# Kernel optimization log

Measured on AMD Instinct MI355X. Metric: run time of the kernel, lower is better.

Reference implementation:

```python
import jax, jax.numpy as jnp
import numpy as np

D = 768
H = 8
HD = D // H
MLP = 3072
EPS = 1e-5


def _ln(x, g, b):
    mu = jnp.mean(x, axis=-1, keepdims=True)
    var = jnp.var(x, axis=-1, keepdims=True)
    return (x - mu) * jax.lax.rsqrt(var + EPS) * g + b


def setup_inputs() -> dict:
    key = jax.random.key(0)
    ks = jax.random.split(key, 20)
    B, N = 4, 2048
    s = 0.02
    inp = {
        "x": jax.random.normal(ks[0], (B, N, D), jnp.float32),
        "position_bias": jax.random.normal(ks[1], (N, N), jnp.float32),
        "wq": jax.random.normal(ks[2], (D, D), jnp.float32) * s,
        "bq": jnp.zeros((D,), jnp.float32),
        "wk": jax.random.normal(ks[3], (D, D), jnp.float32) * s,
        "bk": jnp.zeros((D,), jnp.float32),
        "wv": jax.random.normal(ks[4], (D, D), jnp.float32) * s,
        "bv": jnp.zeros((D,), jnp.float32),
        "wo": jax.random.normal(ks[5], (D, D), jnp.float32) * s,
        "bo": jnp.zeros((D,), jnp.float32),
        "g1": jnp.ones((D,), jnp.float32),
        "b1": jnp.zeros((D,), jnp.float32),
        "g2": jnp.ones((D,), jnp.float32),
        "b2": jnp.zeros((D,), jnp.float32),
        "w_ff1": jax.random.normal(ks[6], (D, MLP), jnp.float32) * s,
        "b_ff1": jnp.zeros((MLP,), jnp.float32),
        "w_ff2": jax.random.normal(ks[7], (MLP, D), jnp.float32) * s,
        "b_ff2": jnp.zeros((D,), jnp.float32),
    }
    return inp


def reference(x, position_bias, wq, bq, wk, bk, wv, bv, wo, bo, g1, b1, g2, b2, w_ff1, b_ff1, w_ff2, b_ff2):
    B, N, _ = x.shape
    scale = HD ** -0.5
    # pre-norm attention
    n1 = _ln(x, g1, b1)
    q = (n1 @ wq + bq).reshape(B, N, H, HD).transpose(0, 2, 1, 3)
    k = (n1 @ wk + bk).reshape(B, N, H, HD).transpose(0, 2, 1, 3)
    v = (n1 @ wv + bv).reshape(B, N, H, HD).transpose(0, 2, 1, 3)
    attn = jnp.einsum('bhqd,bhkd->bhqk', q, k) * scale  # [B,H,N,N]
    attn = attn + position_bias[None, None, :, :]
    attn = jax.nn.softmax(attn, axis=-1)
    out = jnp.einsum('bhqk,bhkd->bhqd', attn, v)
    out = out.transpose(0, 2, 1, 3).reshape(B, N, D)
    out = out @ wo + bo
    x = x + out
    # pre-norm GELU MLP (exact erf gelu, torch default)
    n2 = _ln(x, g2, b2)
    h = jax.nn.gelu(n2 @ w_ff1 + b_ff1, approximate=False)
    x = x + (h @ w_ff2 + b_ff2)
    return x
```

## Files before the change

kernel.cpp:

```cpp
#include <hip/hip_runtime.h>
#include <hip/hip_bf16.h>

#define D 768
#define H 8
#define HD 96
#define MLP 3072
#define NB 2048
#define BATCH 4

typedef __attribute__((ext_vector_type(8))) short short8;
typedef __attribute__((ext_vector_type(4))) short short4v;
typedef __attribute__((ext_vector_type(4))) float f32x4;
typedef __attribute__((ext_vector_type(16))) float f32x16;
typedef __attribute__((ext_vector_type(4))) int int4v;

typedef const __attribute__((address_space(1))) unsigned int gu32;
typedef __attribute__((address_space(3))) unsigned int lu32;

__device__ inline void gload16(const void* g, void* l){
  __builtin_amdgcn_global_load_lds((gu32*)g, (lu32*)l, 16, 0, 0);
}

__device__ inline short f2b(float f){
  __hip_bfloat16 h = __float2bfloat16(f);
  return *reinterpret_cast<short*>(&h);
}
__device__ inline float b2f(short s){
  return __uint_as_float(((unsigned)(unsigned short)s) << 16);
}
__device__ inline float fexp2(float x){ return __builtin_amdgcn_exp2f(x); }

__device__ inline unsigned cvtpk(float lo, float hi){
  unsigned r;
  asm volatile("v_cvt_pk_bf16_f32 %0, %1, %2" : "=v"(r) : "v"(lo), "v"(hi));
  return r;
}

__global__ __launch_bounds__(256) void wtrans(const float* __restrict__ in, short* __restrict__ out, int K, int Nc){
  __shared__ float tile[32][33];
  int bk = blockIdx.x, bn = blockIdx.y;
  int tx = threadIdx.x & 31, ty = threadIdx.x >> 5;
  #pragma unroll
  for (int i=0;i<4;++i)
    tile[ty + i*8][tx] = in[(size_t)(bk*32 + ty + i*8)*Nc + bn*32 + tx];
  __syncthreads();
  #pragma unroll
  for (int i=0;i<4;++i)
    out[(size_t)(bn*32 + ty + i*8)*K + bk*32 + tx] = f2b(tile[tx][ty + i*8]);
}

__global__ __launch_bounds__(256) void bias_cat(const float* __restrict__ bq, const float* __restrict__ bk,
                                                const float* __restrict__ bv, float* __restrict__ o){
  int i = blockIdx.x*256 + threadIdx.x;
  if (i < 768){ o[i]=bq[i]; o[768+i]=bk[i]; o[1536+i]=bv[i]; }
}

__global__ __launch_bounds__(256) void pb_reorg(const float* __restrict__ pb, short* __restrict__ pbT){
  int qt = blockIdx.x, kb = blockIdx.y;
  int t = threadIdx.x;
  int l = t >> 2;
  int vbase = (t & 3) * 8;
  int q = qt*32 + (l & 31);
  int hi = l >> 5;
  const float L2E = 1.4426950408889634f;
  short8 o;
  #pragma unroll
  for (int j=0;j<8;++j){
    int v = vbase + j;
    int r = v & 15, tile = v >> 4;
    int k = kb*64 + tile*32 + 8*(r>>2) + (r&3) + 4*hi;
    o[j] = f2b(pb[(size_t)q*NB + k] * L2E);
  }
  *(short8*)&pbT[(((size_t)(qt*32 + kb))*64 + l)*32 + vbase] = o;
}

__global__ __launch_bounds__(256) void ln_k(const float* __restrict__ X, const float* __restrict__ gg,
                                            const float* __restrict__ bb, short* __restrict__ out){
  int row = blockIdx.x, t = threadIdx.x;
  const float* x = X + (size_t)row*D;
  float v0=x[t], v1=x[t+256], v2=x[t+512];
  float s=v0+v1+v2, ss=v0*v0+v1*v1+v2*v2;
  #pragma unroll
  for (int m=1;m<64;m<<=1){ s += __shfl_xor(s,m); ss += __shfl_xor(ss,m); }
  __shared__ float red[8];
  int w=t>>6, lane=t&63;
  if (!lane){ red[w]=s; red[4+w]=ss; }
  __syncthreads();
  s = red[0]+red[1]+red[2]+red[3];
  ss = red[4]+red[5]+red[6]+red[7];
  float mu = s*(1.f/768.f);
  float inv = rsqrtf(ss*(1.f/768.f) - mu*mu + 1e-5f);
  short* o = out + (size_t)row*D;
  o[t]     = f2b((v0-mu)*inv*gg[t]     + bb[t]);
  o[t+256] = f2b((v1-mu)*inv*gg[t+256] + bb[t+256]);
  o[t+512] = f2b((v2-mu)*inv*gg[t+512] + bb[t+512]);
}

template<int MODE>
__global__ __launch_bounds__(256) void gemm_bt(
    const short* __restrict__ A, const short* __restrict__ Bt,
    const float* __restrict__ bias, const float* __restrict__ resid,
    void* __restrict__ Cout, int Nc, int K)
{
  __shared__ __align__(16) short As[3][128][32];
  __shared__ __align__(16) short Bs[3][128][32];
  int m0 = blockIdx.x*128, n0 = blockIdx.y*128;
  int t = threadIdx.x;
  int lane = t & 63, w = t >> 6;
  int wm = w >> 1, wn = w & 1;
  int r = lane & 15, g = lane >> 4;
  const short* aSrc = A  + (size_t)(m0 + (t>>2))*K + (t&3)*8;
  const short* bSrc = Bt + (size_t)(n0 + (t>>2))*K + (t&3)*8;
  size_t rowK64 = (size_t)64*K;
  int dstOff = w*1024;
  f32x4 acc[4][4] = {};
  int nst = K >> 5;
  auto stage = [&](int u, int buf){
    char* ab = (char*)As + buf*8192;
    char* bb = (char*)Bs + buf*8192;
    int kt = u*32;
    gload16(aSrc + kt,          ab + dstOff);
    gload16(aSrc + kt + rowK64, ab + 4096 + dstOff);
    gload16(bSrc + kt,          bb + dstOff);
    gload16(bSrc + kt + rowK64, bb + 4096 + dstOff);
  };
  stage(0,0); stage(1,1);
  int cur = 0;
  for (int it=0; it<nst; ++it){
    if (it < nst-1) asm volatile("s_waitcnt vmcnt(4)" ::: "memory");
    else            asm volatile("s_waitcnt vmcnt(0)" ::: "memory");
    __builtin_amdgcn_s_barrier();
    __builtin_amdgcn_sched_barrier(0);
    if (it+2 < nst){
      int sb = cur+2; if (sb>=3) sb-=3;
      stage(it+2, sb);
    }
    short8 af[4], bfr[4];
    #pragma unroll
    for (int i=0;i<4;++i){
      af[i]  = *(const short8*)&As[cur][wm*64 + i*16 + r][g*8];
      bfr[i] = *(const short8*)&Bs[cur][wn*64 + i*16 + r][g*8];
    }
    #pragma unroll
    for (int i=0;i<4;++i)
      #pragma unroll
      for (int j=0;j<4;++j)
        acc[i][j] = __builtin_amdgcn_mfma_f32_16x16x32_bf16(af[i], bfr[j], acc[i][j], 0,0,0);
    cur = cur+1; if (cur>=3) cur-=3;
  }
  #pragma unroll
  for (int i=0;i<4;++i){
    #pragma unroll
    for (int j=0;j<4;++j){
      int col = n0 + wn*64 + j*16 + r;
      float bv = bias[col];
      #pragma unroll
      for (int q=0;q<4;++q){
        int row = m0 + wm*64 + i*16 + g*4 + q;
        size_t idx = (size_t)row*Nc + col;
        float val = acc[i][j][q] + bv;
        if constexpr (MODE==0){
          ((short*)Cout)[idx] = f2b(val);
        } else if constexpr (MODE==2){
          float ge = 0.5f*val*(1.f + erff(val*0.70710678118654752f));
          ((short*)Cout)[idx] = f2b(ge);
        }
      }
    }
  }
}

template<int MODE>
__global__ __launch_bounds__(256) void gemm64(
    const short* __restrict__ A, const short* __restrict__ Bt,
    const float* __restrict__ bias, const float* __restrict__ resid,
    void* __restrict__ Cout, int Nc, int K)
{
  __shared__ __align__(16) short As[3][64][32];
  __shared__ __align__(16) short Bs[3][128][32];
  int m0 = blockIdx.x*64, n0 = blockIdx.y*128;
  int t = threadIdx.x;
  int lane = t & 63, w = t >> 6;
  int r = lane & 15, g = lane >> 4;
  const short* aSrc = A  + (size_t)(m0 + (t>>2))*K + (t&3)*8;
  const short* bSrc = Bt + (size_t)(n0 + (t>>2))*K + (t&3)*8;
  size_t rowK64 = (size_t)64*K;
  int dstOff = w*1024;
  f32x4 acc[4][2] = {};
  int nst = K >> 5;
  auto stage = [&](int u, int buf){
    char* ab = (char*)As + buf*4096;
    char* bb = (char*)Bs + buf*8192;
    int kt = u*32;
    gload16(aSrc + kt,          ab + dstOff);
    gload16(bSrc + kt,          bb + dstOff);
    gload16(bSrc + kt + rowK64, bb + 4096 + dstOff);
  };
  stage(0,0); stage(1,1);
  int cur = 0;
  for (int it=0; it<nst; ++it){
    if (it < nst-1) asm volatile("s_waitcnt vmcnt(3)" ::: "memory");
    else            asm volatile("s_waitcnt vmcnt(0)" ::: "memory");
    __builtin_amdgcn_s_barrier();
    __builtin_amdgcn_sched_barrier(0);
    if (it+2 < nst){
      int sb = cur+2; if (sb>=3) sb-=3;
      stage(it+2, sb);
    }
    short8 af[4], bfr[2];
    #pragma unroll
    for (int i=0;i<4;++i) af[i] = *(const short8*)&As[cur][i*16 + r][g*8];
    #pragma unroll
    for (int j=0;j<2;++j) bfr[j] = *(const short8*)&Bs[cur][w*32 + j*16 + r][g*8];
    #pragma unroll
    for (int i=0;i<4;++i)
      #pragma unroll
      for (int j=0;j<2;++j)
        acc[i][j] = __builtin_amdgcn_mfma_f32_16x16x32_bf16(af[i], bfr[j], acc[i][j], 0,0,0);
    cur = cur+1; if (cur>=3) cur-=3;
  }
  #pragma unroll
  for (int i=0;i<4;++i){
    #pragma unroll
    for (int j=0;j<2;++j){
      int col = n0 + w*32 + j*16 + r;
      #pragma unroll
      for (int q=0;q<4;++q){
        int row = m0 + i*16 + g*4 + q;
        if constexpr (MODE==1){
          size_t idx = (size_t)row*Nc + col;
          ((float*)Cout)[idx] = acc[i][j][q] + bias[col] + resid[idx];
        } else {
          int hh = row / 96, hd = row - hh*96;
          int bb = col >> 11, nn = col & 2047;
          size_t idx = ((size_t)((bb*8 + hh)*96 + hd))*2048 + nn;
          ((short*)Cout)[idx] = f2b(acc[i][j][q] + bias[row]);
        }
      }
    }
  }
}

__global__ __launch_bounds__(512, 1) void attn_k(const short* __restrict__ qkv, const short* __restrict__ v_t,
                                                 const short* __restrict__ pbT, short* __restrict__ aout){
  int bx = blockIdx.x;
  int h = bx & 7, b = (bx>>3)&3, qb = bx>>5;
  int t = threadIdx.x, l = t & 63, w = t >> 6;
  int l31 = l & 31, hi = l >> 5, l7 = l & 7;
  __shared__ __align__(16) short Ks[2][64][128];
  __shared__ __align__(16) short Vs[2][96][64];
  const float SCALE2 = 0.10206207261596575f * 1.4426950408889634f;

  int qRow = qb*256 + w*32 + l31;
  const short* qg = qkv + (size_t)(b*NB + qRow)*1536 + h*HD;
  short8 qa[6];
  #pragma unroll
  for (int ds=0; ds<6; ++ds)
    qa[ds] = *(const short8*)&qg[ds*16 + hi*8];

  f32x16 oacc[3] = {};
  float m_run = -3.0e38f, l_run = 0.f;

  int r0 = t/12,        c0 = t%12;
  int s1 = 512 + t;
  int r1 = s1/12,       c1 = s1%12;
  int ldsK0 = r0*128 + (c0 ^ (r0&7))*8;
  int ldsK1 = r1*128 + (c1 ^ (r1&7))*8;
  const short* kgB = qkv + (size_t)(b*NB)*1536 + 768 + h*HD;
  bool wlow = (t < 256);
  int vr0 = t>>3,  vc0 = t&7;
  int vr1 = (512+t)>>3, vc1 = (512+t)&7;
  const short* vgB = v_t + (size_t)((b*H+h)*HD)*NB;
  const short* vsrc0 = vgB + (size_t)vr0*NB + (vc0 ^ (vr0&7))*8;
  const short* vsrc1 = vgB + (size_t)vr1*NB + (vc1 ^ (vr1&7))*8;
  const short* pbB = pbT + (((size_t)((qb*8 + w)*32))*64 + l)*32;

  {
    short8 ka = *(const short8*)&kgB[(size_t)r0*1536 + c0*8];
    short* ks0 = &Ks[0][0][0];
    *(short8*)(ks0 + ldsK0) = ka;
    if (wlow){
      short8 kb = *(const short8*)&kgB[(size_t)r1*1536 + c1*8];
      *(short8*)(ks0 + ldsK1) = kb;
    }
    gload16(vsrc0, (char*)Vs + w*1024);
    if (wlow) gload16(vsrc1, (char*)Vs + 8192 + w*1024);
  }
  __syncthreads();

  for (int kt=0; kt<32; ++kt){
    int cur = kt & 1;
    int kbase = kt*64;
    int kb2 = (kt < 31) ? (kbase + 64) : kbase;
    short8 kra = *(const short8*)&kgB[(size_t)(kb2 + r0)*1536 + c0*8];
    short8 krb = {};
    if (wlow) krb = *(const short8*)&kgB[(size_t)(kb2 + r1)*1536 + c1*8];
    const short* pbk = pbB + kt*2048;
    short8 pbr0 = *(const short8*)&pbk[0];
    short8 pbr1 = *(const short8*)&pbk[8];
    short8 pbr2 = *(const short8*)&pbk[16];
    short8 pbr3 = *(const short8*)&pbk[24];
    if (kt < 31){
      char* vbd = (char*)Vs + (cur^1)*12288;
      gload16(vsrc0 + kbase + 64, vbd + w*1024);
      if (wlow) gload16(vsrc1 + kbase + 64, vbd + 8192 + w*1024);
    }

    f32x16 sacc[2] = {};
    __builtin_amdgcn_s_setprio(1);
    #pragma unroll
    for (int tt=0; tt<2; ++tt){
      #pragma unroll
      for (int ds=0; ds<6; ++ds){
        short8 kf = *(const short8*)&Ks[cur][tt*32 + l31][((ds*2 + hi) ^ l7)*8];
        sacc[tt] = __builtin_amdgcn_mfma_f32_32x32x16_bf16(kf, qa[ds], sacc[tt], 0,0,0);
      }
    }
    __builtin_amdgcn_s_setprio(0);

    float vals[2][16];
    #pragma unroll
    for (int tt=0; tt<2; ++tt)
      #pragma unroll
      for (int r=0; r<16; ++r){
        int v = tt*16 + r;
        short pv = (v<8)?pbr0[v]:(v<16)?pbr1[v-8]:(v<24)?pbr2[v-16]:pbr3[v-24];
        vals[tt][r] = fmaf(sacc[tt][r], SCALE2, b2f(pv));
      }
    float pm = vals[0][0];
    #pragma unroll
    for (int tt=0; tt<2; ++tt)
      #pragma unroll
      for (int r=0; r<16; ++r) pm = fmaxf(pm, vals[tt][r]);
    pm = fmaxf(pm, __shfl_xor(pm, 32));
    if (__any(pm - m_run > 8.f)){
      float mn = fmaxf(m_run, pm);
      float f = fexp2(m_run - mn);
      l_run *= f; m_run = mn;
      int fi = __float_as_int(f);
      #pragma unroll
      for (int reg=0; reg<16; ++reg){
        int q = (reg&3) + 8*(reg>>2) + 4*hi;
        float fr = __int_as_float(__builtin_amdgcn_ds_bpermute(q<<2, fi));
        oacc[0][reg] *= fr; oacc[1][reg] *= fr; oacc[2][reg] *= fr;
      }
    }
    float p[2][16];
    float rs = 0.f;
    #pragma unroll
    for (int tt=0; tt<2; ++tt)
      #pragma unroll
      for (int r=0; r<16; ++r){
        p[tt][r] = fexp2(vals[tt][r] - m_run);
        rs += p[tt][r];
      }
    rs += __shfl_xor(rs, 32);
    l_run += rs;

    short8 pa[4];
    #pragma unroll
    for (int ks=0; ks<4; ++ks){
      int tt = ks>>1;
      int rb = (ks&1)*8;
      unsigned G0a = cvtpk(p[tt][rb+0], p[tt][rb+1]);
      unsigned G0b = cvtpk(p[tt][rb+2], p[tt][rb+3]);
      unsigned G1a = cvtpk(p[tt][rb+4], p[tt][rb+5]);
      unsigned G1b = cvtpk(p[tt][rb+6], p[tt][rb+7]);
      unsigned sG0a = (unsigned)__shfl_xor((int)G0a, 32);
      unsigned sG0b = (unsigned)__shfl_xor((int)G0b, 32);
      unsigned sG1a = (unsigned)__shfl_xor((int)G1a, 32);
      unsigned sG1b = (unsigned)__shfl_xor((int)G1b, 32);
      int4v wv;
      wv[0] = hi ? (int)sG1a : (int)G0a;
      wv[1] = hi ? (int)sG1b : (int)G0b;
      wv[2] = hi ? (int)G1a  : (int)sG0a;
      wv[3] = hi ? (int)G1b  : (int)sG0b;
      pa[ks] = __builtin_bit_cast(short8, wv);
    }

    __builtin_amdgcn_s_setprio(1);
    #pragma unroll
    for (int dt=0; dt<3; ++dt){
      #pragma unroll
      for (int ks=0; ks<4; ++ks){
        short8 vb = *(const short8*)&Vs[cur][dt*32 + l31][((ks*2 + hi) ^ l7)*8];
        oacc[dt] = __builtin_amdgcn_mfma_f32_32x32x16_bf16(pa[ks], vb, oacc[dt], 0,0,0);
      }
    }
    __builtin_amdgcn_s_setprio(0);

    if (kt < 31){
      short* ksn = &Ks[cur^1][0][0];
      *(short8*)(ksn + ldsK0) = kra;
      if (wlow) *(short8*)(ksn + ldsK1) = krb;
      __syncthreads();
    }
  }

  float inv_self = 1.f / l_run;
  int ii = __float_as_int(inv_self);
  #pragma unroll
  for (int reg=0; reg<16; ++reg){
    int q = (reg&3) + 8*(reg>>2) + 4*hi;
    float invq = __int_as_float(__builtin_amdgcn_ds_bpermute(q<<2, ii));
    int rowg = b*NB + qb*256 + w*32 + q;
    #pragma unroll
    for (int dt=0; dt<3; ++dt){
      int col = h*HD + dt*32 + l31;
      aout[(size_t)rowg*D + col] = f2b(oacc[dt][reg] * invq);
    }
  }
}

extern "C" void kernel_launch(void* const* d_in, const int* in_sizes, int n_in,
                              void* d_out, int out_size, void* d_ws, size_t ws_size,
                              hipStream_t stream){
  const float* x   = (const float*)d_in[0];
  const float* pb  = (const float*)d_in[1];
  const float* wq  = (const float*)d_in[2];
  const float* bq  = (const float*)d_in[3];
  const float* wk  = (const float*)d_in[4];
  const float* bk  = (const float*)d_in[5];
  const float* wv  = (const float*)d_in[6];
  const float* bv  = (const float*)d_in[7];
  const float* wo  = (const float*)d_in[8];
  const float* bo  = (const float*)d_in[9];
  const float* g1  = (const float*)d_in[10];
  const float* b1  = (const float*)d_in[11];
  const float* g2  = (const float*)d_in[12];
  const float* b2  = (const float*)d_in[13];
  const float* wf1 = (const float*)d_in[14];
  const float* bf1 = (const float*)d_in[15];
  const float* wf2 = (const float*)d_in[16];
  const float* bf2 = (const float*)d_in[17];
  float* out = (float*)d_out;

  char* p = (char*)d_ws;
  auto alloc = [&](size_t bytes){ char* q = p; p += (bytes + 255) & ~(size_t)255; return q; };
  short* wqkv_t = (short*)alloc((size_t)2304*768*2);
  short* wo_t   = (short*)alloc((size_t)768*768*2);
  short* w1_t   = (short*)alloc((size_t)3072*768*2);
  short* w2_t   = (short*)alloc((size_t)768*3072*2);
  float* bqkv   = (float*)alloc(2304*4);
  short* pbT    = (short*)alloc((size_t)2048*2048*2);
  float* x1     = (float*)alloc((size_t)8192*768*4);
  short* n2     = (short*)alloc((size_t)8192*768*2);
  short* n1     = (short*)alloc((size_t)8192*768*2);
  short* qkv    = (short*)alloc((size_t)8192*1536*2);
  short* v_t    = (short*)alloc((size_t)32*96*2048*2);
  short* hbuf   = n1;
  short* attn_o = n1;
  short* wv_t   = wqkv_t + (size_t)2*768*768;

  wtrans<<<dim3(24,24),256,0,stream>>>(wq, wqkv_t,           768, 768);
  wtrans<<<dim3(24,24),256,0,stream>>>(wk, wqkv_t + 768*768, 768, 768);
  wtrans<<<dim3(24,24),256,0,stream>>>(wv, wv_t,             768, 768);
  wtrans<<<dim3(24,24),256,0,stream>>>(wo, wo_t, 768, 768);
  wtrans<<<dim3(24,96),256,0,stream>>>(wf1, w1_t, 768, 3072);
  wtrans<<<dim3(96,24),256,0,stream>>>(wf2, w2_t, 3072, 768);
  bias_cat<<<3,256,0,stream>>>(bq,bk,bv,bqkv);
  pb_reorg<<<dim3(64,32),256,0,stream>>>(pb, pbT);
  ln_k<<<8192,256,0,stream>>>(x, g1, b1, n1);
  gemm_bt<0><<<dim3(64,12),256,0,stream>>>(n1, wqkv_t, bqkv, nullptr, qkv, 1536, 768);
  gemm64<5><<<dim3(12,64),256,0,stream>>>(wv_t, n1, bv, nullptr, v_t, 0, 768);
  attn_k<<<256,512,0,stream>>>(qkv, v_t, pbT, attn_o);
  gemm64<1><<<dim3(128,6),256,0,stream>>>(attn_o, wo_t, bo, x, x1, 768, 768);
  ln_k<<<8192,256,0,stream>>>(x1, g2, b2, n2);
  gemm_bt<2><<<dim3(64,24),256,0,stream>>>(n2, w1_t, bf1, nullptr, hbuf, 3072, 768);
  gemm64<1><<<dim3(128,6),256,0,stream>>>(hbuf, w2_t, bf2, x1, out, 768, 3072);
}
```

Baseline: 318.7 us.

## Process two key tiles per barrier and load K via async global-to-LDS

Restructures the attention kernel's main loop to handle two 64-key tiles per iteration, with 128 keys per double-buffered stage, halving the number of block barriers. K tiles are now fetched with global_load_lds instead of register loads followed by LDS stores. The K swizzle moves to the global source address, and QK MFMAs for both tiles are issued back to back before the softmax work. This doubles LDS use and raises register pressure because four score accumulators are live at once.

```diff
diff --git a/kernel.cpp b/kernel.cpp
--- a/kernel.cpp
+++ b/kernel.cpp
@@ -247,8 +247,10 @@
   int h = bx & 7, b = (bx>>3)&3, qb = bx>>5;
   int t = threadIdx.x, l = t & 63, w = t >> 6;
   int l31 = l & 31, hi = l >> 5, l7 = l & 7;
-  __shared__ __align__(16) short Ks[2][64][128];
-  __shared__ __align__(16) short Vs[2][96][64];
+  __shared__ __align__(16) short Ks[2][2][64][128];
+  __shared__ __align__(16) short Vs[2][2][96][64];
+  char* KsB = (char*)Ks;
+  char* VsB = (char*)Vs;
   const float SCALE2 = 0.10206207261596575f * 1.4426950408889634f;
 
   int qRow = qb*256 + w*32 + l31;
@@ -261,139 +263,219 @@
   f32x16 oacc[3] = {};
   float m_run = -3.0e38f, l_run = 0.f;
 
-  int r0 = t/12,        c0 = t%12;
-  int s1 = 512 + t;
-  int r1 = s1/12,       c1 = s1%12;
-  int ldsK0 = r0*128 + (c0 ^ (r0&7))*8;
-  int ldsK1 = r1*128 + (c1 ^ (r1&7))*8;
   const short* kgB = qkv + (size_t)(b*NB)*1536 + 768 + h*HD;
-  bool wlow = (t < 256);
-  int vr0 = t>>3,  vc0 = t&7;
-  int vr1 = (512+t)>>3, vc1 = (512+t)&7;
+  const short* kSrc[4]; int kDoff[4];
+  #pragma unroll
+  for (int j=0;j<4;++j){
+    int s = j*512 + t;
+    int tile = s >> 10, si = s & 1023;
+    int r = si >> 4, c = si & 15;
+    kSrc[j] = kgB + (size_t)(tile*64 + r)*1536 + ((c ^ (r&7))*8);
+    kDoff[j] = tile*16384 + (j&1)*8192 + w*1024;
+  }
   const short* vgB = v_t + (size_t)((b*H+h)*HD)*NB;
-  const short* vsrc0 = vgB + (size_t)vr0*NB + (vc0 ^ (vr0&7))*8;
-  const short* vsrc1 = vgB + (size_t)vr1*NB + (vc1 ^ (vr1&7))*8;
+  const short* vSrc[3]; int vDoff[3];
+  #pragma unroll
+  for (int j=0;j<3;++j){
+    int tile, within, doff;
+    if (j==0){ tile=0; within=t;            doff = w*1024; }
+    else if (j==1){
+      if (t < 256){ tile=0; within=512+t;   doff = 8192 + w*1024; }
+      else        { tile=1; within=t-256;   doff = 12288 + (w-4)*1024; }
+    } else { tile=1; within=256+t;          doff = 12288 + 4096 + w*1024; }
+    int vr = within >> 3, vc = within & 7;
+    vSrc[j] = vgB + (size_t)vr*NB + ((vc ^ (vr&7))*8) + tile*64;
+    vDoff[j] = doff;
+  }
   const short* pbB = pbT + (((size_t)((qb*8 + w)*32))*64 + l)*32;
 
-  {
-    short8 ka = *(const short8*)&kgB[(size_t)r0*1536 + c0*8];
-    short* ks0 = &Ks[0][0][0];
-    *(short8*)(ks0 + ldsK0) = ka;
-    if (wlow){
-      short8 kb = *(const short8*)&kgB[(size_t)r1*1536 + c1*8];
-      *(short8*)(ks0 + ldsK1) = kb;
-    }
-    gload16(vsrc0, (char*)Vs + w*1024);
-    if (wlow) gload16(vsrc1, (char*)Vs + 8192 + w*1024);
-  }
-  __syncthreads();
-
-  for (int kt=0; kt<32; ++kt){
-    int cur = kt & 1;
-    int kbase = kt*64;
-    int kb2 = (kt < 31) ? (kbase + 64) : kbase;
-    short8 kra = *(const short8*)&kgB[(size_t)(kb2 + r0)*1536 + c0*8];
-    short8 krb = {};
-    if (wlow) krb = *(const short8*)&kgB[(size_t)(kb2 + r1)*1536 + c1*8];
-    const short* pbk = pbB + kt*2048;
-    short8 pbr0 = *(const short8*)&pbk[0];
-    short8 pbr1 = *(const short8*)&pbk[8];
-    short8 pbr2 = *(const short8*)&pbk[16];
-    short8 pbr3 = *(const short8*)&pbk[24];
-    if (kt < 31){
-      char* vbd = (char*)Vs + (cur^1)*12288;
-      gload16(vsrc0 + kbase + 64, vbd + w*1024);
-      if (wlow) gload16(vsrc1 + kbase + 64, vbd + 8192 + w*1024);
-    }
-
-    f32x16 sacc[2] = {};
+  #pragma unroll
+  for (int j=0;j<4;++j) gload16(kSrc[j], KsB + kDoff[j]);
+  #pragma unroll
+  for (int j=0;j<3;++j) gload16(vSrc[j], VsB + vDoff[j]);
+
+  for (int p=0; p<16; ++p){
+    int cb = p & 1;
+    __syncthreads();
+    if (p < 15){
+      int nb = (p+1) & 1;
+      size_t pk = (size_t)(p+1)*128;
+      #pragma unroll
+      for (int j=0;j<4;++j) gload16(kSrc[j] + pk*1536, KsB + nb*32768 + kDoff[j]);
+      #pragma unroll
+      for (int j=0;j<3;++j) gload16(vSrc[j] + pk,      VsB + nb*24576 + vDoff[j]);
+    }
+    const short* pbk = pbB + (size_t)(p*2)*2048;
+    short8 pA0 = *(const short8*)&pbk[0];
+    short8 pA1 = *(const short8*)&pbk[8];
+    short8 pA2 = *(const short8*)&pbk[16];
+    short8 pA3 = *(const short8*)&pbk[24];
+    short8 pB0 = *(const short8*)&pbk[2048];
+    short8 pB1 = *(const short8*)&pbk[2056];
+    short8 pB2 = *(const short8*)&pbk[2064];
+    short8 pB3 = *(const short8*)&pbk[2072];
+
+    const short* KsA  = (const short*)(KsB + cb*32768);
+    const short* KsBt = (const short*)(KsB + cb*32768 + 16384);
+    const short* VsA  = (const short*)(VsB + cb*24576);
+    const short* VsBt = (const short*)(VsB + cb*24576 + 12288);
+
+    f32x16 sA0={}, sA1={}, sB0={}, sB1={};
     __builtin_amdgcn_s_setprio(1);
     #pragma unroll
-    for (int tt=0; tt<2; ++tt){
-      #pragma unroll
-      for (int ds=0; ds<6; ++ds){
-        short8 kf = *(const short8*)&Ks[cur][tt*32 + l31][((ds*2 + hi) ^ l7)*8];
-        sacc[tt] = __builtin_amdgcn_mfma_f32_32x32x16_bf16(kf, qa[ds], sacc[tt], 0,0,0);
-      }
+    for (int ds=0; ds<6; ++ds){
+      short8 kf0 = *(const short8*)&KsA[(size_t)(l31)*128      + (((ds*2 + hi) ^ l7)*8)];
+      short8 kf1 = *(const short8*)&KsA[(size_t)(32 + l31)*128 + (((ds*2 + hi) ^ l7)*8)];
+      sA0 = __builtin_amdgcn_mfma_f32_32x32x16_bf16(kf0, qa[ds], sA0, 0,0,0);
+      sA1 = __builtin_amdgcn_mfma_f32_32x32x16_bf16(kf1, qa[ds], sA1, 0,0,0);
+    }
+    #pragma unroll
+    for (int ds=0; ds<6; ++ds){
+      short8 kf0 = *(const short8*)&KsBt[(size_t)(l31)*128      + (((ds*2 + hi) ^ l7)*8)];
+      short8 kf1 = *(const short8*)&KsBt[(size_t)(32 + l31)*128 + (((ds*2 + hi) ^ l7)*8)];
+      sB0 = __builtin_amdgcn_mfma_f32_32x32x16_bf16(kf0, qa[ds], sB0, 0,0,0);
+      sB1 = __builtin_amdgcn_mfma_f32_32x32x16_bf16(kf1, qa[ds], sB1, 0,0,0);
     }
     __builtin_amdgcn_s_setprio(0);
 
-    float vals[2][16];
-    #pragma unroll
-    for (int tt=0; tt<2; ++tt)
+    {
+      float vals[2][16];
       #pragma unroll
       for (int r=0; r<16; ++r){
-        int v = tt*16 + r;
-        short pv = (v<8)?pbr0[v]:(v<16)?pbr1[v-8]:(v<24)?pbr2[v-16]:pbr3[v-24];
-        vals[tt][r] = fmaf(sacc[tt][r], SCALE2, b2f(pv));
-      }
-    float pm = vals[0][0];
-    #pragma unroll
-    for (int tt=0; tt<2; ++tt)
-      #pragma unroll
-      for (int r=0; r<16; ++r) pm = fmaxf(pm, vals[tt][r]);
-    pm = fmaxf(pm, __shfl_xor(pm, 32));
-    if (__any(pm - m_run > 8.f)){
-      float mn = fmaxf(m_run, pm);
-      float f = fexp2(m_run - mn);
-      l_run *= f; m_run = mn;
-      int fi = __float_as_int(f);
-      #pragma unroll
-      for (int reg=0; reg<16; ++reg){
-        int q = (reg&3) + 8*(reg>>2) + 4*hi;
-        float fr = __int_as_float(__builtin_amdgcn_ds_bpermute(q<<2, fi));
-        oacc[0][reg] *= fr; oacc[1][reg] *= fr; oacc[2][reg] *= fr;
-      }
-    }
-    float p[2][16];
-    float rs = 0.f;
-    #pragma unroll
-    for (int tt=0; tt<2; ++tt)
+        short pv0 = (r<8)?pA0[r]:pA1[r-8];
+        short pv1 = (r<8)?pA2[r]:pA3[r-8];
+        vals[0][r] = fmaf(sA0[r], SCALE2, b2f(pv0));
+        vals[1][r] = fmaf(sA1[r], SCALE2, b2f(pv1));
+      }
+      float pm = vals[0][0];
+      #pragma unroll
+      for (int tt=0; tt<2; ++tt)
+        #pragma unroll
+        for (int r=0; r<16; ++r) pm = fmaxf(pm, vals[tt][r]);
+      pm = fmaxf(pm, __shfl_xor(pm, 32));
+      if (__any(pm - m_run > 8.f)){
+        float mn = fmaxf(m_run, pm);
+        float f = fexp2(m_run - mn);
+        l_run *= f; m_run = mn;
+        int fi = __float_as_int(f);
+        #pragma unroll
+        for (int reg=0; reg<16; ++reg){
+          int q = (reg&3) + 8*(reg>>2) + 4*hi;
+          float fr = __int_as_float(__builtin_amdgcn_ds_bpermute(q<<2, fi));
+          oacc[0][reg] *= fr; oacc[1][reg] *= fr; oacc[2][reg] *= fr;
+        }
+      }
+      float pp[2][16];
+      float rs = 0.f;
+      #pragma unroll
+      for (int tt=0; tt<2; ++tt)
+        #pragma unroll
+        for (int r=0; r<16; ++r){
+          pp[tt][r] = fexp2(vals[tt][r] - m_run);
+          rs += pp[tt][r];
+        }
+      rs += __shfl_xor(rs, 32);
+      l_run += rs;
+      short8 pa[4];
+      #pragma unroll
+      for (int ks=0; ks<4; ++ks){
+        int tt = ks>>1;
+        int rb = (ks&1)*8;
+        unsigned G0a = cvtpk(pp[tt][rb+0], pp[tt][rb+1]);
+        unsigned G0b = cvtpk(pp[tt][rb+2], pp[tt][rb+3]);
+        unsigned G1a = cvtpk(pp[tt][rb+4], pp[tt][rb+5]);
+        unsigned G1b = cvtpk(pp[tt][rb+6], pp[tt][rb+7]);
+        unsigned sG0a = (unsigned)__shfl_xor((int)G0a, 32);
+        unsigned sG0b = (unsigned)__shfl_xor((int)G0b, 32);
+        unsigned sG1a = (unsigned)__shfl_xor((int)G1a, 32);
+        unsigned sG1b = (unsigned)__shfl_xor((int)G1b, 32);
+        int4v wv;
+        wv[0] = hi ? (int)sG1a : (int)G0a;
+        wv[1] = hi ? (int)sG1b : (int)G0b;
+        wv[2] = hi ? (int)G1a  : (int)sG0a;
+        wv[3] = hi ? (int)G1b  : (int)sG0b;
+        pa[ks] = __builtin_bit_cast(short8, wv);
+      }
+      __builtin_amdgcn_s_setprio(1);
+      #pragma unroll
+      for (int dt=0; dt<3; ++dt){
+        #pragma unroll
+        for (int ks=0; ks<4; ++ks){
+          short8 vb = *(const short8*)&VsA[(size_t)(dt*32 + l31)*64 + (((ks*2 + hi) ^ l7)*8)];
+          oacc[dt] = __builtin_amdgcn_mfma_f32_32x32x16_bf16(pa[ks], vb, oacc[dt], 0,0,0);
+        }
+      }
+      __builtin_amdgcn_s_setprio(0);
+    }
+
+    {
+      float vals[2][16];
       #pragma unroll
       for (int r=0; r<16; ++r){
-        p[tt][r] = fexp2(vals[tt][r] - m_run);
-        rs += p[tt][r];
-      }
-    rs += __shfl_xor(rs, 32);
-    l_run += rs;
-
-    short8 pa[4];
-    #pragma unroll
-    for (int ks=0; ks<4; ++ks){
-      int tt = ks>>1;
-      int rb = (ks&1)*8;
-      unsigned G0a = cvtpk(p[tt][rb+0], p[tt][rb+1]);
-      unsigned G0b = cvtpk(p[tt][rb+2], p[tt][rb+3]);
-      unsigned G1a = cvtpk(p[tt][rb+4], p[tt][rb+5]);
-      unsigned G1b = cvtpk(p[tt][rb+6], p[tt][rb+7]);
-      unsigned sG0a = (unsigned)__shfl_xor((int)G0a, 32);
-      unsigned sG0b = (unsigned)__shfl_xor((int)G0b, 32);
-      unsigned sG1a = (unsigned)__shfl_xor((int)G1a, 32);
-      unsigned sG1b = (unsigned)__shfl_xor((int)G1b, 32);
-      int4v wv;
-      wv[0] = hi ? (int)sG1a : (int)G0a;
-      wv[1] = hi ? (int)sG1b : (int)G0b;
-      wv[2] = hi ? (int)G1a  : (int)sG0a;
-      wv[3] = hi ? (int)G1b  : (int)sG0b;
-      pa[ks] = __builtin_bit_cast(short8, wv);
-    }
-
-    __builtin_amdgcn_s_setprio(1);
-    #pragma unroll
-    for (int dt=0; dt<3; ++dt){
+        short pv0 = (r<8)?pB0[r]:pB1[r-8];
+        short pv1 = (r<8)?pB2[r]:pB3[r-8];
+        vals[0][r] = fmaf(sB0[r], SCALE2, b2f(pv0));
+        vals[1][r] = fmaf(sB1[r], SCALE2, b2f(pv1));
+      }
+      float pm = vals[0][0];
+      #pragma unroll
+      for (int tt=0; tt<2; ++tt)
+        #pragma unroll
+        for (int r=0; r<16; ++r) pm = fmaxf(pm, vals[tt][r]);
+      pm = fmaxf(pm, __shfl_xor(pm, 32));
+      if (__any(pm - m_run > 8.f)){
+        float mn = fmaxf(m_run, pm);
+        float f = fexp2(m_run - mn);
+        l_run *= f; m_run = mn;
+        int fi = __float_as_int(f);
+        #pragma unroll
+        for (int reg=0; reg<16; ++reg){
+          int q = (reg&3) + 8*(reg>>2) + 4*hi;
+          float fr = __int_as_float(__builtin_amdgcn_ds_bpermute(q<<2, fi));
+          oacc[0][reg] *= fr; oacc[1][reg] *= fr; oacc[2][reg] *= fr;
+        }
+      }
+      float pp[2][16];
+      float rs = 0.f;
+      #pragma unroll
+      for (int tt=0; tt<2; ++tt)
+        #pragma unroll
+        for (int r=0; r<16; ++r){
+          pp[tt][r] = fexp2(vals[tt][r] - m_run);
+          rs += pp[tt][r];
+        }
+      rs += __shfl_xor(rs, 32);
+      l_run += rs;
+      short8 pa[4];
       #pragma unroll
       for (int ks=0; ks<4; ++ks){
-        short8 vb = *(const short8*)&Vs[cur][dt*32 + l31][((ks*2 + hi) ^ l7)*8];
-        oacc[dt] = __builtin_amdgcn_mfma_f32_32x32x16_bf16(pa[ks], vb, oacc[dt], 0,0,0);
-      }
-    }
-    __builtin_amdgcn_s_setprio(0);
-
-    if (kt < 31){
-      short* ksn = &Ks[cur^1][0][0];
-      *(short8*)(ksn + ldsK0) = kra;
-      if (wlow) *(short8*)(ksn + ldsK1) = krb;
-      __syncthreads();
+        int tt = ks>>1;
+        int rb = (ks&1)*8;
+        unsigned G0a = cvtpk(pp[tt][rb+0], pp[tt][rb+1]);
+        unsigned G0b = cvtpk(pp[tt][rb+2], pp[tt][rb+3]);
+        unsigned G1a = cvtpk(pp[tt][rb+4], pp[tt][rb+5]);
+        unsigned G1b = cvtpk(pp[tt][rb+6], pp[tt][rb+7]);
+        unsigned sG0a = (unsigned)__shfl_xor((int)G0a, 32);
+        unsigned sG0b = (unsigned)__shfl_xor((int)G0b, 32);
+        unsigned sG1a = (unsigned)__shfl_xor((int)G1a, 32);
+        unsigned sG1b = (unsigned)__shfl_xor((int)G1b, 32);
+        int4v wv;
+        wv[0] = hi ? (int)sG1a : (int)G0a;
+        wv[1] = hi ? (int)sG1b : (int)G0b;
+        wv[2] = hi ? (int)G1a  : (int)sG0a;
+        wv[3] = hi ? (int)G1b  : (int)sG0b;
+        pa[ks] = __builtin_bit_cast(short8, wv);
+      }
+      __builtin_amdgcn_s_setprio(1);
+      #pragma unroll
+      for (int dt=0; dt<3; ++dt){
+        #pragma unroll
+        for (int ks=0; ks<4; ++ks){
+          short8 vb = *(const short8*)&VsBt[(size_t)(dt*32 + l31)*64 + (((ks*2 + hi) ^ l7)*8)];
+          oacc[dt] = __builtin_amdgcn_mfma_f32_32x32x16_bf16(pa[ks], vb, oacc[dt], 0,0,0);
+        }
+      }
+      __builtin_amdgcn_s_setprio(0);
     }
   }
 
```

After: 326.3 us. 1.02x slower.
